# Kernel tuning notes

Hardware: AMD Instinct MI355X
Metric: run time of the kernel (lower is better)

## Reference

```python
import jax, jax.numpy as jnp
import numpy as np

EMBED = 1024
HEAD = 128

def setup_inputs() -> dict:
    key = jax.random.key(0)
    k1, k2, k3, k4 = jax.random.split(key, 4)
    x = jax.random.normal(k1, (8, 2048, EMBED), dtype=jnp.float32)
    s = 1.0 / np.sqrt(EMBED)
    Wk = jax.random.normal(k2, (EMBED, HEAD), dtype=jnp.float32) * s
    Wq = jax.random.normal(k3, (EMBED, HEAD), dtype=jnp.float32) * s
    Wv = jax.random.normal(k4, (EMBED, HEAD), dtype=jnp.float32) * s
    return {"x": x, "Wk": Wk, "Wq": Wq, "Wv": Wv}

def reference(x, Wk, Wq, Wv):
    # x: [B,T,E]; projections: [B,T,H]
    k = x @ Wk
    q = x @ Wq
    v = x @ Wv
    T = x.shape[1]
    # NOTE: original scales by 1/sqrt(embedding_size), not head_size
    scale = 1.0 / jnp.sqrt(jnp.asarray(EMBED, dtype=x.dtype))
    scores = jnp.einsum('bth,bsh->bts', q, k) * scale  # [B,T,T]
    causal = jnp.tril(jnp.ones((T, T), dtype=bool))
    scores = jnp.where(causal, scores, -jnp.inf)
    attn = jax.nn.softmax(scores, axis=-1)
    return jnp.einsum('bts,bsh->bth', attn, v)
```

## Files before the change

kernel.cpp:

```cpp
#include <hip/hip_runtime.h>
#include <math.h>

typedef short bf16x2 __attribute__((ext_vector_type(2)));
typedef short bf16x4 __attribute__((ext_vector_type(4)));
typedef short bf16x8 __attribute__((ext_vector_type(8)));
typedef float f32x4 __attribute__((ext_vector_type(4)));

#define EMBED 1024
#define HEAD 128
#define BATCH 8
#define SEQ 2048

__device__ __forceinline__ short f2bf(float f) {
  union { float f; unsigned u; } v;
  v.f = f;
  unsigned r = v.u + 0x7fffu + ((v.u >> 16) & 1u);
  return (short)(r >> 16);
}

__device__ __forceinline__ void async_copy16(const void* g, void* l) {
#if __has_builtin(__builtin_amdgcn_global_load_lds)
  __builtin_amdgcn_global_load_lds(
      (const __attribute__((address_space(1))) unsigned int*)g,
      (__attribute__((address_space(3))) unsigned int*)l, 16, 0, 0);
#else
  *(f32x4*)l = *(const f32x4*)g;
#endif
}

__global__ __launch_bounds__(256) void wtrans_kernel(
    const float* __restrict__ Wq, const float* __restrict__ Wk,
    const float* __restrict__ Wv, short* __restrict__ WT) {
  __shared__ float tile[32][33];
  int kt = blockIdx.x * 32;
  int ht = blockIdx.y * 32;
  int mtx = blockIdx.z;
  const float* W = (mtx == 0) ? Wq : ((mtx == 1) ? Wk : Wv);
  float scale = (mtx == 0) ? (1.4426950408889634f / 32.0f) : 1.0f;
  int tc = threadIdx.x & 31;
  int tr = threadIdx.x >> 5;
#pragma unroll
  for (int i = 0; i < 4; i++) {
    int r = tr + i * 8;
    tile[r][tc] = W[(size_t)(kt + r) * HEAD + ht + tc];
  }
  __syncthreads();
#pragma unroll
  for (int i = 0; i < 4; i++) {
    int r = tr + i * 8;
    WT[(size_t)(mtx * HEAD + ht + r) * EMBED + kt + tc] = f2bf(tile[tc][r] * scale);
  }
}

__global__ __launch_bounds__(256, 3) void proj_kernel(
    const float* __restrict__ x, const short* __restrict__ WT,
    short* __restrict__ q, short* __restrict__ k, short* __restrict__ vT) {
  __shared__ __align__(16) short As[2][64 * 72];
  __shared__ __align__(16) short Bs[2][64 * 128];
  int tid = threadIdx.x;
  int w = tid >> 6, lane = tid & 63, quad = lane >> 4, sub = lane & 15;
  int mw = w & 1, nw = w >> 1;
  int bx = blockIdx.x;
  int nt = bx % 3;
  int mt = bx / 3;
  int m0 = mt * 64;
  int bb = m0 >> 11;
  int t0 = m0 & 2047;

  int arow = tid >> 2;
  int akq = (tid & 3) * 16;
  const float* xbase = x + (size_t)(m0 + arow) * EMBED + akq;
  int aoff = arow * 72 + akq;

  const short* wsrc[4];
#pragma unroll
  for (int j = 0; j < 4; j++) {
    int cc = j * 256 + tid;
    wsrc[j] = WT + (size_t)(nt * 128 + (cc & 127)) * EMBED + (cc >> 7) * 8;
  }

  f32x4 acc[2][4];
#pragma unroll
  for (int am = 0; am < 2; am++)
#pragma unroll
    for (int an = 0; an < 4; an++) acc[am][an] = (f32x4)(0.0f);

  {
    f32x4 x0 = *(const f32x4*)(xbase + 0);
    f32x4 x1 = *(const f32x4*)(xbase + 4);
    f32x4 x2 = *(const f32x4*)(xbase + 8);
    f32x4 x3 = *(const f32x4*)(xbase + 12);
    bf16x8 w0, w1;
    w0[0]=f2bf(x0[0]); w0[1]=f2bf(x0[1]); w0[2]=f2bf(x0[2]); w0[3]=f2bf(x0[3]);
    w0[4]=f2bf(x1[0]); w0[5]=f2bf(x1[1]); w0[6]=f2bf(x1[2]); w0[7]=f2bf(x1[3]);
    w1[0]=f2bf(x2[0]); w1[1]=f2bf(x2[1]); w1[2]=f2bf(x2[2]); w1[3]=f2bf(x2[3]);
    w1[4]=f2bf(x3[0]); w1[5]=f2bf(x3[1]); w1[6]=f2bf(x3[2]); w1[7]=f2bf(x3[3]);
    *(bf16x8*)&As[0][aoff] = w0;
    *(bf16x8*)&As[0][aoff + 8] = w1;
#pragma unroll
    for (int j = 0; j < 4; j++) async_copy16(wsrc[j], &Bs[0][(j * 256 + tid) * 8]);
  }
  f32x4 xr0 = *(const f32x4*)(xbase + 64);
  f32x4 xr1 = *(const f32x4*)(xbase + 68);
  f32x4 xr2 = *(const f32x4*)(xbase + 72);
  f32x4 xr3 = *(const f32x4*)(xbase + 76);

  for (int it = 0; it < 16; it++) {
    int cur = it & 1;
    __syncthreads();
    if (it < 15) {
      int nxt = cur ^ 1;
      bf16x8 w0, w1;
      w0[0]=f2bf(xr0[0]); w0[1]=f2bf(xr0[1]); w0[2]=f2bf(xr0[2]); w0[3]=f2bf(xr0[3]);
      w0[4]=f2bf(xr1[0]); w0[5]=f2bf(xr1[1]); w0[6]=f2bf(xr1[2]); w0[7]=f2bf(xr1[3]);
      w1[0]=f2bf(xr2[0]); w1[1]=f2bf(xr2[1]); w1[2]=f2bf(xr2[2]); w1[3]=f2bf(xr2[3]);
      w1[4]=f2bf(xr3[0]); w1[5]=f2bf(xr3[1]); w1[6]=f2bf(xr3[2]); w1[7]=f2bf(xr3[3]);
      *(bf16x8*)&As[nxt][aoff] = w0;
      *(bf16x8*)&As[nxt][aoff + 8] = w1;
      int kb1 = (it + 1) * 64;
#pragma unroll
      for (int j = 0; j < 4; j++)
        async_copy16(wsrc[j] + kb1, &Bs[nxt][(j * 256 + tid) * 8]);
      if (it < 14) {
        int kb2 = (it + 2) * 64;
        xr0 = *(const f32x4*)(xbase + kb2);
        xr1 = *(const f32x4*)(xbase + kb2 + 4);
        xr2 = *(const f32x4*)(xbase + kb2 + 8);
        xr3 = *(const f32x4*)(xbase + kb2 + 12);
      }
    }
#pragma unroll
    for (int ks = 0; ks < 2; ks++) {
      bf16x8 a0 = *(const bf16x8*)&As[cur][(mw * 32 + sub) * 72 + ks * 32 + quad * 8];
      bf16x8 a1 = *(const bf16x8*)&As[cur][(mw * 32 + 16 + sub) * 72 + ks * 32 + quad * 8];
#pragma unroll
      for (int an = 0; an < 4; an++) {
        bf16x8 bb = *(const bf16x8*)&Bs[cur][((ks * 4 + quad) * 128 + nw * 64 + an * 16 + sub) * 8];
        acc[0][an] = __builtin_amdgcn_mfma_f32_16x16x32_bf16(a0, bb, acc[0][an], 0, 0, 0);
        acc[1][an] = __builtin_amdgcn_mfma_f32_16x16x32_bf16(a1, bb, acc[1][an], 0, 0, 0);
      }
    }
  }

  if (nt < 2) {
    short* dst = (nt == 0) ? q : k;
#pragma unroll
    for (int am = 0; am < 2; am++)
#pragma unroll
      for (int an = 0; an < 4; an++) {
        int col = nw * 64 + an * 16 + sub;
#pragma unroll
        for (int r = 0; r < 4; r++) {
          int m = m0 + mw * 32 + am * 16 + quad * 4 + r;
          dst[(size_t)m * HEAD + col] = f2bf(acc[am][an][r]);
        }
      }
  } else {
    short* vls = &As[0][0];
    __syncthreads();
#pragma unroll
    for (int am = 0; am < 2; am++)
#pragma unroll
      for (int an = 0; an < 4; an++) {
        int h = nw * 64 + an * 16 + sub;
        int m = mw * 32 + am * 16 + quad * 4;
        bf16x4 pv;
#pragma unroll
        for (int r = 0; r < 4; r++) pv[r] = f2bf(acc[am][an][r]);
        *(bf16x4*)&vls[h * 72 + m] = pv;
      }
    __syncthreads();
    int h = tid >> 1, seg = tid & 1;
    bf16x8 v0 = *(const bf16x8*)&vls[h * 72 + seg * 32];
    bf16x8 v1 = *(const bf16x8*)&vls[h * 72 + seg * 32 + 8];
    bf16x8 v2 = *(const bf16x8*)&vls[h * 72 + seg * 32 + 16];
    bf16x8 v3 = *(const bf16x8*)&vls[h * 72 + seg * 32 + 24];
    short* dp = vT + (size_t)(bb * HEAD + h) * SEQ + t0 + seg * 32;
    *(bf16x8*)(dp) = v0;
    *(bf16x8*)(dp + 8) = v1;
    *(bf16x8*)(dp + 16) = v2;
    *(bf16x8*)(dp + 24) = v3;
  }
}

__global__ __launch_bounds__(256, 4) void attn_kernel(
    const short* __restrict__ q, const short* __restrict__ k,
    const short* __restrict__ vT, float* __restrict__ o_acc,
    float* __restrict__ l_acc) {
  __shared__ __align__(16) short Kb[2][4096];
  __shared__ __align__(16) short Vb[2][4096];
  __shared__ __align__(16) short Pb[4][2][16 * 40];
  int tid = threadIdx.x;
  int w = tid >> 6, lane = tid & 63, quad = lane >> 4, sub = lane & 15;
  int bx = blockIdx.x;
  int b = bx & 7;
  int v = 79 - (bx >> 3);
  int qt, c;
  if (v < 8)       { qt = v;                               c = 0; }
  else if (v < 24) { int i2 = v - 8;  qt = 8  + (i2 >> 1); c = i2 & 1; }
  else if (v < 48) { int i2 = v - 24; qt = 16 + i2 / 3;    c = i2 % 3; }
  else             { int i2 = v - 48; qt = 24 + (i2 >> 2); c = i2 & 3; }
  int q0 = qt * 64;
  int kb0 = c * 512;
  int len = min(512, q0 + 64 - kb0);
  int ntiles = len >> 5;

  const short* kp = k + (size_t)b * SEQ * HEAD;
  const short* vp = vT + (size_t)b * HEAD * SEQ;
  int cc0 = tid, cc1 = tid + 256;

  bf16x8 qf[4];
  const short* qrow = q + (size_t)(b * SEQ + q0 + w * 16 + sub) * HEAD + quad * 8;
#pragma unroll
  for (int kc = 0; kc < 4; kc++) qf[kc] = *(const bf16x8*)(qrow + kc * 32);

  f32x4 o[8];
#pragma unroll
  for (int h = 0; h < 8; h++) o[h] = (f32x4)(0.0f);
  float l[4] = {0.0f, 0.0f, 0.0f, 0.0f};
  int wrow = q0 + w * 16;
  int qrq = wrow + quad * 4;

  async_copy16(kp + (size_t)(kb0 + (cc0 & 31)) * HEAD + (cc0 >> 5) * 8, &Kb[0][cc0 * 8]);
  async_copy16(kp + (size_t)(kb0 + (cc1 & 31)) * HEAD + (cc1 >> 5) * 8, &Kb[0][cc1 * 8]);
  async_copy16(vp + (size_t)(cc0 & 127) * SEQ + kb0 + (cc0 >> 7) * 8, &Vb[0][cc0 * 8]);
  async_copy16(vp + (size_t)(cc1 & 127) * SEQ + kb0 + (cc1 >> 7) * 8, &Vb[0][cc1 * 8]);

  for (int j = 0; j < ntiles; j++) {
    int kb = kb0 + j * 32;
    int cur = j & 1;
    __syncthreads();
    if (j + 1 < ntiles) {
      int nxt = cur ^ 1;
      int kb1 = kb + 32;
      async_copy16(kp + (size_t)(kb1 + (cc0 & 31)) * HEAD + (cc0 >> 5) * 8, &Kb[nxt][cc0 * 8]);
      async_copy16(kp + (size_t)(kb1 + (cc1 & 31)) * HEAD + (cc1 >> 5) * 8, &Kb[nxt][cc1 * 8]);
      async_copy16(vp + (size_t)(cc0 & 127) * SEQ + kb1 + (cc0 >> 7) * 8, &Vb[nxt][cc0 * 8]);
      async_copy16(vp + (size_t)(cc1 & 127) * SEQ + kb1 + (cc1 >> 7) * 8, &Vb[nxt][cc1 * 8]);
    }
    f32x4 s0 = (f32x4)(0.0f), s1 = (f32x4)(0.0f);
#pragma unroll
    for (int kk = 0; kk < 4; kk++) {
      bf16x8 f0 = *(const bf16x8*)&Kb[cur][((kk * 4 + quad) * 32 + sub) * 8];
      bf16x8 f1 = *(const bf16x8*)&Kb[cur][((kk * 4 + quad) * 32 + 16 + sub) * 8];
      s0 = __builtin_amdgcn_mfma_f32_16x16x32_bf16(qf[kk], f0, s0, 0, 0, 0);
      s1 = __builtin_amdgcn_mfma_f32_16x16x32_bf16(qf[kk], f1, s1, 0, 0, 0);
    }
    bool edge = (kb + 31 > wrow);
    float e0[4], e1[4];
#pragma unroll
    for (int r = 0; r < 4; r++) {
      e0[r] = __builtin_amdgcn_exp2f(s0[r]);
      e1[r] = __builtin_amdgcn_exp2f(s1[r]);
    }
    if (edge) {
#pragma unroll
      for (int r = 0; r < 4; r++) {
        if (kb + sub > qrq + r) e0[r] = 0.0f;
        if (kb + 16 + sub > qrq + r) e1[r] = 0.0f;
      }
    }
    short* pw = &Pb[w][cur][0];
#pragma unroll
    for (int r = 0; r < 4; r++) {
      l[r] += e0[r] + e1[r];
      pw[(quad * 4 + r) * 40 + sub] = f2bf(e0[r]);
      pw[(quad * 4 + r) * 40 + sub + 16] = f2bf(e1[r]);
    }
    bf16x8 pa = *(const bf16x8*)&pw[sub * 40 + quad * 8];
#pragma unroll
    for (int h8 = 0; h8 < 8; h8++) {
      bf16x8 vf = *(const bf16x8*)&Vb[cur][(quad * 128 + h8 * 16 + sub) * 8];
      o[h8] = __builtin_amdgcn_mfma_f32_16x16x32_bf16(pa, vf, o[h8], 0, 0, 0);
    }
  }

  float* ob = o_acc + (size_t)(b * SEQ + qrq) * HEAD + sub;
#pragma unroll
  for (int r = 0; r < 4; r++)
#pragma unroll
    for (int h8 = 0; h8 < 8; h8++)
      unsafeAtomicAdd(ob + (size_t)r * HEAD + h8 * 16, o[h8][r]);
#pragma unroll
  for (int r = 0; r < 4; r++) {
#pragma unroll
    for (int off = 1; off < 16; off <<= 1) l[r] += __shfl_xor(l[r], off);
  }
  if (sub == 0) {
#pragma unroll
    for (int r = 0; r < 4; r++)
      unsafeAtomicAdd(&l_acc[b * SEQ + qrq + r], l[r]);
  }
}

__global__ __launch_bounds__(256) void norm_kernel(
    float* __restrict__ o, const float* __restrict__ l_acc) {
  int idx = blockIdx.x * 256 + threadIdx.x;
  f32x4 v = ((const f32x4*)o)[idx];
  float inv = 1.0f / l_acc[idx >> 5];
  v[0] *= inv; v[1] *= inv; v[2] *= inv; v[3] *= inv;
  ((f32x4*)o)[idx] = v;
}

extern "C" void kernel_launch(void* const* d_in, const int* in_sizes, int n_in,
                              void* d_out, int out_size, void* d_ws, size_t ws_size,
                              hipStream_t stream) {
  const float* x  = (const float*)d_in[0];
  const float* Wk = (const float*)d_in[1];
  const float* Wq = (const float*)d_in[2];
  const float* Wv = (const float*)d_in[3];
  char* ws = (char*)d_ws;
  short* WT    = (short*)(ws);
  short* vT    = (short*)(ws + (size_t)1  * (1 << 20));
  short* q     = (short*)(ws + (size_t)5  * (1 << 20));
  short* k     = (short*)(ws + (size_t)9  * (1 << 20));
  float* l_acc = (float*)(ws + (size_t)13 * (1 << 20));
  float* out   = (float*)d_out;

  hipMemsetAsync(out, 0, (size_t)BATCH * SEQ * HEAD * sizeof(float), stream);
  hipMemsetAsync(l_acc, 0, (size_t)BATCH * SEQ * sizeof(float), stream);
  wtrans_kernel<<<dim3(32, 4, 3), 256, 0, stream>>>(Wq, Wk, Wv, WT);
  proj_kernel<<<dim3(768), 256, 0, stream>>>(x, WT, q, k, vT);
  attn_kernel<<<dim3(640), 256, 0, stream>>>(q, k, vT, out, l_acc);
  norm_kernel<<<dim3(2048), 256, 0, stream>>>(out, l_acc);
}
```

Measured before the change: 177.0 us.

## Fuse QKV projection into one wide tile and load V directly from global

The projection kernel now computes all three Q/K/V outputs per 64-row tile, using 512-thread blocks over 384 columns. Each x tile is read and converted to bf16 once instead of three times, at the cost of only 256 blocks at one block per CU and a larger LDS footprint. Separately, the attention kernel drops the LDS staging buffer for V and loads V fragments straight from global memory into registers each iteration. This removes LDS traffic and space but exposes global load latency inside the loop without async prefetch.

```diff
diff --git a/kernel.cpp b/kernel.cpp
--- a/kernel.cpp
+++ b/kernel.cpp
@@ -52,134 +52,111 @@
   }
 }
 
-__global__ __launch_bounds__(256, 3) void proj_kernel(
+__global__ __launch_bounds__(512, 1) void proj_kernel(
     const float* __restrict__ x, const short* __restrict__ WT,
     short* __restrict__ q, short* __restrict__ k, short* __restrict__ vT) {
-  __shared__ __align__(16) short As[2][64 * 72];
-  __shared__ __align__(16) short Bs[2][64 * 128];
+  __shared__ __align__(16) short As[2][512 * 8];
+  __shared__ __align__(16) short Bs[2][3072 * 8];
   int tid = threadIdx.x;
   int w = tid >> 6, lane = tid & 63, quad = lane >> 4, sub = lane & 15;
-  int mw = w & 1, nw = w >> 1;
-  int bx = blockIdx.x;
-  int nt = bx % 3;
-  int mt = bx / 3;
-  int m0 = mt * 64;
-  int bb = m0 >> 11;
-  int t0 = m0 & 2047;
-
-  int arow = tid >> 2;
-  int akq = (tid & 3) * 16;
-  const float* xbase = x + (size_t)(m0 + arow) * EMBED + akq;
-  int aoff = arow * 72 + akq;
-
-  const short* wsrc[4];
-#pragma unroll
-  for (int j = 0; j < 4; j++) {
-    int cc = j * 256 + tid;
-    wsrc[j] = WT + (size_t)(nt * 128 + (cc & 127)) * EMBED + (cc >> 7) * 8;
-  }
-
-  f32x4 acc[2][4];
+  int mw = w >> 2, nw = w & 3;
+  int m0 = blockIdx.x * 64;
+  int bb = m0 >> 11, t0 = m0 & 2047;
+
+  int arow = tid & 63, akq = tid >> 6;
+  const float* xbase = x + (size_t)(m0 + arow) * EMBED + akq * 8;
+
+  const short* wsrc[6];
+  int bdst[6];
+#pragma unroll
+  for (int j = 0; j < 6; j++) {
+    int c = j * 512 + tid;
+    int kq = c / 384, n = c - kq * 384;
+    wsrc[j] = WT + (size_t)n * EMBED + kq * 8;
+    bdst[j] = c * 8;
+  }
+
+  f32x4 acc[2][6];
 #pragma unroll
   for (int am = 0; am < 2; am++)
 #pragma unroll
-    for (int an = 0; an < 4; an++) acc[am][an] = (f32x4)(0.0f);
+    for (int an = 0; an < 6; an++) acc[am][an] = (f32x4)(0.0f);
 
   {
-    f32x4 x0 = *(const f32x4*)(xbase + 0);
+    f32x4 x0 = *(const f32x4*)(xbase);
     f32x4 x1 = *(const f32x4*)(xbase + 4);
-    f32x4 x2 = *(const f32x4*)(xbase + 8);
-    f32x4 x3 = *(const f32x4*)(xbase + 12);
-    bf16x8 w0, w1;
-    w0[0]=f2bf(x0[0]); w0[1]=f2bf(x0[1]); w0[2]=f2bf(x0[2]); w0[3]=f2bf(x0[3]);
-    w0[4]=f2bf(x1[0]); w0[5]=f2bf(x1[1]); w0[6]=f2bf(x1[2]); w0[7]=f2bf(x1[3]);
-    w1[0]=f2bf(x2[0]); w1[1]=f2bf(x2[1]); w1[2]=f2bf(x2[2]); w1[3]=f2bf(x2[3]);
-    w1[4]=f2bf(x3[0]); w1[5]=f2bf(x3[1]); w1[6]=f2bf(x3[2]); w1[7]=f2bf(x3[3]);
-    *(bf16x8*)&As[0][aoff] = w0;
-    *(bf16x8*)&As[0][aoff + 8] = w1;
-#pragma unroll
-    for (int j = 0; j < 4; j++) async_copy16(wsrc[j], &Bs[0][(j * 256 + tid) * 8]);
+    bf16x8 a8;
+    a8[0]=f2bf(x0[0]); a8[1]=f2bf(x0[1]); a8[2]=f2bf(x0[2]); a8[3]=f2bf(x0[3]);
+    a8[4]=f2bf(x1[0]); a8[5]=f2bf(x1[1]); a8[6]=f2bf(x1[2]); a8[7]=f2bf(x1[3]);
+    *(bf16x8*)&As[0][tid * 8] = a8;
+#pragma unroll
+    for (int j = 0; j < 6; j++) async_copy16(wsrc[j], &Bs[0][bdst[j]]);
   }
   f32x4 xr0 = *(const f32x4*)(xbase + 64);
   f32x4 xr1 = *(const f32x4*)(xbase + 68);
-  f32x4 xr2 = *(const f32x4*)(xbase + 72);
-  f32x4 xr3 = *(const f32x4*)(xbase + 76);
 
   for (int it = 0; it < 16; it++) {
     int cur = it & 1;
     __syncthreads();
     if (it < 15) {
       int nxt = cur ^ 1;
-      bf16x8 w0, w1;
-      w0[0]=f2bf(xr0[0]); w0[1]=f2bf(xr0[1]); w0[2]=f2bf(xr0[2]); w0[3]=f2bf(xr0[3]);
-      w0[4]=f2bf(xr1[0]); w0[5]=f2bf(xr1[1]); w0[6]=f2bf(xr1[2]); w0[7]=f2bf(xr1[3]);
-      w1[0]=f2bf(xr2[0]); w1[1]=f2bf(xr2[1]); w1[2]=f2bf(xr2[2]); w1[3]=f2bf(xr2[3]);
-      w1[4]=f2bf(xr3[0]); w1[5]=f2bf(xr3[1]); w1[6]=f2bf(xr3[2]); w1[7]=f2bf(xr3[3]);
-      *(bf16x8*)&As[nxt][aoff] = w0;
-      *(bf16x8*)&As[nxt][aoff + 8] = w1;
+      bf16x8 a8;
+      a8[0]=f2bf(xr0[0]); a8[1]=f2bf(xr0[1]); a8[2]=f2bf(xr0[2]); a8[3]=f2bf(xr0[3]);
+      a8[4]=f2bf(xr1[0]); a8[5]=f2bf(xr1[1]); a8[6]=f2bf(xr1[2]); a8[7]=f2bf(xr1[3]);
+      *(bf16x8*)&As[nxt][tid * 8] = a8;
       int kb1 = (it + 1) * 64;
 #pragma unroll
-      for (int j = 0; j < 4; j++)
-        async_copy16(wsrc[j] + kb1, &Bs[nxt][(j * 256 + tid) * 8]);
+      for (int j = 0; j < 6; j++) async_copy16(wsrc[j] + kb1, &Bs[nxt][bdst[j]]);
       if (it < 14) {
-        int kb2 = (it + 2) * 64;
-        xr0 = *(const f32x4*)(xbase + kb2);
-        xr1 = *(const f32x4*)(xbase + kb2 + 4);
-        xr2 = *(const f32x4*)(xbase + kb2 + 8);
-        xr3 = *(const f32x4*)(xbase + kb2 + 12);
+        xr0 = *(const f32x4*)(xbase + (it + 2) * 64);
+        xr1 = *(const f32x4*)(xbase + (it + 2) * 64 + 4);
       }
     }
 #pragma unroll
     for (int ks = 0; ks < 2; ks++) {
-      bf16x8 a0 = *(const bf16x8*)&As[cur][(mw * 32 + sub) * 72 + ks * 32 + quad * 8];
-      bf16x8 a1 = *(const bf16x8*)&As[cur][(mw * 32 + 16 + sub) * 72 + ks * 32 + quad * 8];
-#pragma unroll
-      for (int an = 0; an < 4; an++) {
-        bf16x8 bb = *(const bf16x8*)&Bs[cur][((ks * 4 + quad) * 128 + nw * 64 + an * 16 + sub) * 8];
-        acc[0][an] = __builtin_amdgcn_mfma_f32_16x16x32_bf16(a0, bb, acc[0][an], 0, 0, 0);
-        acc[1][an] = __builtin_amdgcn_mfma_f32_16x16x32_bf16(a1, bb, acc[1][an], 0, 0, 0);
+      int kq = ks * 4 + quad;
+      bf16x8 a0 = *(const bf16x8*)&As[cur][(kq * 64 + mw * 32 + sub) * 8];
+      bf16x8 a1 = *(const bf16x8*)&As[cur][(kq * 64 + mw * 32 + 16 + sub) * 8];
+#pragma unroll
+      for (int an = 0; an < 6; an++) {
+        bf16x8 b8 = *(const bf16x8*)&Bs[cur][(kq * 384 + nw * 96 + an * 16 + sub) * 8];
+        acc[0][an] = __builtin_amdgcn_mfma_f32_16x16x32_bf16(a0, b8, acc[0][an], 0, 0, 0);
+        acc[1][an] = __builtin_amdgcn_mfma_f32_16x16x32_bf16(a1, b8, acc[1][an], 0, 0, 0);
       }
     }
   }
 
-  if (nt < 2) {
-    short* dst = (nt == 0) ? q : k;
-#pragma unroll
-    for (int am = 0; am < 2; am++)
-#pragma unroll
-      for (int an = 0; an < 4; an++) {
-        int col = nw * 64 + an * 16 + sub;
+  short* vls = &Bs[0][0];
+#pragma unroll
+  for (int am = 0; am < 2; am++)
+#pragma unroll
+    for (int an = 0; an < 6; an++) {
+      int nbt = nw * 6 + an;
+      if (nbt < 16) {
+        short* dst = (nbt < 8) ? q : k;
+        int col = (nbt & 7) * 16 + sub;
 #pragma unroll
         for (int r = 0; r < 4; r++) {
           int m = m0 + mw * 32 + am * 16 + quad * 4 + r;
           dst[(size_t)m * HEAD + col] = f2bf(acc[am][an][r]);
         }
-      }
-  } else {
-    short* vls = &As[0][0];
-    __syncthreads();
-#pragma unroll
-    for (int am = 0; am < 2; am++)
-#pragma unroll
-      for (int an = 0; an < 4; an++) {
-        int h = nw * 64 + an * 16 + sub;
+      } else {
+        int h = (nbt - 16) * 16 + sub;
         int m = mw * 32 + am * 16 + quad * 4;
         bf16x4 pv;
 #pragma unroll
         for (int r = 0; r < 4; r++) pv[r] = f2bf(acc[am][an][r]);
         *(bf16x4*)&vls[h * 72 + m] = pv;
       }
-    __syncthreads();
-    int h = tid >> 1, seg = tid & 1;
-    bf16x8 v0 = *(const bf16x8*)&vls[h * 72 + seg * 32];
-    bf16x8 v1 = *(const bf16x8*)&vls[h * 72 + seg * 32 + 8];
-    bf16x8 v2 = *(const bf16x8*)&vls[h * 72 + seg * 32 + 16];
-    bf16x8 v3 = *(const bf16x8*)&vls[h * 72 + seg * 32 + 24];
-    short* dp = vT + (size_t)(bb * HEAD + h) * SEQ + t0 + seg * 32;
-    *(bf16x8*)(dp) = v0;
+    }
+  __syncthreads();
+  {
+    int h = tid >> 2, seg = tid & 3;
+    bf16x8 v0 = *(const bf16x8*)&vls[h * 72 + seg * 16];
+    bf16x8 v1 = *(const bf16x8*)&vls[h * 72 + seg * 16 + 8];
+    short* dp = vT + (size_t)(bb * HEAD + h) * SEQ + t0 + seg * 16;
+    *(bf16x8*)dp = v0;
     *(bf16x8*)(dp + 8) = v1;
-    *(bf16x8*)(dp + 16) = v2;
-    *(bf16x8*)(dp + 24) = v3;
   }
 }
 
@@ -188,7 +165,6 @@
     const short* __restrict__ vT, float* __restrict__ o_acc,
     float* __restrict__ l_acc) {
   __shared__ __align__(16) short Kb[2][4096];
-  __shared__ __align__(16) short Vb[2][4096];
   __shared__ __align__(16) short Pb[4][2][16 * 40];
   int tid = threadIdx.x;
   int w = tid >> 6, lane = tid & 63, quad = lane >> 4, sub = lane & 15;
@@ -206,7 +182,7 @@
   int ntiles = len >> 5;
 
   const short* kp = k + (size_t)b * SEQ * HEAD;
-  const short* vp = vT + (size_t)b * HEAD * SEQ;
+  const short* vbase = vT + (size_t)(b * HEAD + sub) * SEQ + quad * 8;
   int cc0 = tid, cc1 = tid + 256;
 
   bf16x8 qf[4];
@@ -223,8 +199,6 @@
 
   async_copy16(kp + (size_t)(kb0 + (cc0 & 31)) * HEAD + (cc0 >> 5) * 8, &Kb[0][cc0 * 8]);
   async_copy16(kp + (size_t)(kb0 + (cc1 & 31)) * HEAD + (cc1 >> 5) * 8, &Kb[0][cc1 * 8]);
-  async_copy16(vp + (size_t)(cc0 & 127) * SEQ + kb0 + (cc0 >> 7) * 8, &Vb[0][cc0 * 8]);
-  async_copy16(vp + (size_t)(cc1 & 127) * SEQ + kb0 + (cc1 >> 7) * 8, &Vb[0][cc1 * 8]);
 
   for (int j = 0; j < ntiles; j++) {
     int kb = kb0 + j * 32;
@@ -235,9 +209,11 @@
       int kb1 = kb + 32;
       async_copy16(kp + (size_t)(kb1 + (cc0 & 31)) * HEAD + (cc0 >> 5) * 8, &Kb[nxt][cc0 * 8]);
       async_copy16(kp + (size_t)(kb1 + (cc1 & 31)) * HEAD + (cc1 >> 5) * 8, &Kb[nxt][cc1 * 8]);
-      async_copy16(vp + (size_t)(cc0 & 127) * SEQ + kb1 + (cc0 >> 7) * 8, &Vb[nxt][cc0 * 8]);
-      async_copy16(vp + (size_t)(cc1 & 127) * SEQ + kb1 + (cc1 >> 7) * 8, &Vb[nxt][cc1 * 8]);
-    }
+    }
+    bf16x8 vf[8];
+#pragma unroll
+    for (int h8 = 0; h8 < 8; h8++)
+      vf[h8] = *(const bf16x8*)(vbase + (size_t)(h8 * 16) * SEQ + kb);
     f32x4 s0 = (f32x4)(0.0f), s1 = (f32x4)(0.0f);
 #pragma unroll
     for (int kk = 0; kk < 4; kk++) {
@@ -269,10 +245,8 @@
     }
     bf16x8 pa = *(const bf16x8*)&pw[sub * 40 + quad * 8];
 #pragma unroll
-    for (int h8 = 0; h8 < 8; h8++) {
-      bf16x8 vf = *(const bf16x8*)&Vb[cur][(quad * 128 + h8 * 16 + sub) * 8];
-      o[h8] = __builtin_amdgcn_mfma_f32_16x16x32_bf16(pa, vf, o[h8], 0, 0, 0);
-    }
+    for (int h8 = 0; h8 < 8; h8++)
+      o[h8] = __builtin_amdgcn_mfma_f32_16x16x32_bf16(pa, vf[h8], o[h8], 0, 0, 0);
   }
 
   float* ob = o_acc + (size_t)(b * SEQ + qrq) * HEAD + sub;
@@ -320,7 +294,7 @@
   hipMemsetAsync(out, 0, (size_t)BATCH * SEQ * HEAD * sizeof(float), stream);
   hipMemsetAsync(l_acc, 0, (size_t)BATCH * SEQ * sizeof(float), stream);
   wtrans_kernel<<<dim3(32, 4, 3), 256, 0, stream>>>(Wq, Wk, Wv, WT);
-  proj_kernel<<<dim3(768), 256, 0, stream>>>(x, WT, q, k, vT);
+  proj_kernel<<<dim3(256), 512, 0, stream>>>(x, WT, q, k, vT);
   attn_kernel<<<dim3(640), 256, 0, stream>>>(q, k, vT, out, l_acc);
   norm_kernel<<<dim3(2048), 256, 0, stream>>>(out, l_acc);
 }
```

After: 203.9 us. 15.2% more time.

## Split attention KV range into 256-key chunks and regroup projection blocks

Applied to the files above, without the earlier changes.

The attention kernel now splits each query tile's causal key range into 256-key chunks instead of 512, which raises the grid from 640 to 1152 blocks. A closed-form group decode with up to 8 chunks per group replaces the old piecewise mapping, aiming at better load balance and fuller CU occupancy on the causal triangle. The P staging buffer loses its double-buffer dimension, cutting shared memory per block. The projection kernel reorders blocks so that 8 consecutive row tiles share each weight column tile, to improve L2 reuse of the weights. The trade-off is more partial-output atomic traffic into o_acc/l_acc and reuse of a single P buffer per wave across iterations.

```diff
diff --git a/kernel.cpp b/kernel.cpp
--- a/kernel.cpp
+++ b/kernel.cpp
@@ -61,9 +61,11 @@
   int w = tid >> 6, lane = tid & 63, quad = lane >> 4, sub = lane & 15;
   int mw = w & 1, nw = w >> 1;
   int bx = blockIdx.x;
-  int nt = bx % 3;
-  int mt = bx / 3;
-  int m0 = mt * 64;
+  int sup = bx / 24;
+  int rem = bx - sup * 24;
+  int nt = rem >> 3;
+  int s = sup * 8 + (rem & 7);
+  int m0 = s * 64;
   int bb = m0 >> 11;
   int t0 = m0 & 2047;
 
@@ -135,9 +137,9 @@
       bf16x8 a1 = *(const bf16x8*)&As[cur][(mw * 32 + 16 + sub) * 72 + ks * 32 + quad * 8];
 #pragma unroll
       for (int an = 0; an < 4; an++) {
-        bf16x8 bb = *(const bf16x8*)&Bs[cur][((ks * 4 + quad) * 128 + nw * 64 + an * 16 + sub) * 8];
-        acc[0][an] = __builtin_amdgcn_mfma_f32_16x16x32_bf16(a0, bb, acc[0][an], 0, 0, 0);
-        acc[1][an] = __builtin_amdgcn_mfma_f32_16x16x32_bf16(a1, bb, acc[1][an], 0, 0, 0);
+        bf16x8 bb8 = *(const bf16x8*)&Bs[cur][((ks * 4 + quad) * 128 + nw * 64 + an * 16 + sub) * 8];
+        acc[0][an] = __builtin_amdgcn_mfma_f32_16x16x32_bf16(a0, bb8, acc[0][an], 0, 0, 0);
+        acc[1][an] = __builtin_amdgcn_mfma_f32_16x16x32_bf16(a1, bb8, acc[1][an], 0, 0, 0);
       }
     }
   }
@@ -189,20 +191,24 @@
     float* __restrict__ l_acc) {
   __shared__ __align__(16) short Kb[2][4096];
   __shared__ __align__(16) short Vb[2][4096];
-  __shared__ __align__(16) short Pb[4][2][16 * 40];
+  __shared__ __align__(16) short Pb[4][16 * 40];
   int tid = threadIdx.x;
   int w = tid >> 6, lane = tid & 63, quad = lane >> 4, sub = lane & 15;
   int bx = blockIdx.x;
   int b = bx & 7;
-  int v = 79 - (bx >> 3);
-  int qt, c;
-  if (v < 8)       { qt = v;                               c = 0; }
-  else if (v < 24) { int i2 = v - 8;  qt = 8  + (i2 >> 1); c = i2 & 1; }
-  else if (v < 48) { int i2 = v - 24; qt = 16 + i2 / 3;    c = i2 % 3; }
-  else             { int i2 = v - 48; qt = 24 + (i2 >> 2); c = i2 & 3; }
+  int v = 143 - (bx >> 3);
+  int g = 0;
+#pragma unroll
+  for (int gg = 1; gg < 8; gg++)
+    if (v >= 2 * gg * (gg + 1)) g = gg;
+  int r0 = v - 2 * g * (g + 1);
+  int den = g + 1;
+  int qi = r0 / den;
+  int c = r0 - qi * den;
+  int qt = 4 * g + qi;
   int q0 = qt * 64;
-  int kb0 = c * 512;
-  int len = min(512, q0 + 64 - kb0);
+  int kb0 = c * 256;
+  int len = min(256, q0 + 64 - kb0);
   int ntiles = len >> 5;
 
   const short* kp = k + (size_t)b * SEQ * HEAD;
@@ -260,7 +266,7 @@
         if (kb + 16 + sub > qrq + r) e1[r] = 0.0f;
       }
     }
-    short* pw = &Pb[w][cur][0];
+    short* pw = &Pb[w][0];
 #pragma unroll
     for (int r = 0; r < 4; r++) {
       l[r] += e0[r] + e1[r];
@@ -321,6 +327,6 @@
   hipMemsetAsync(l_acc, 0, (size_t)BATCH * SEQ * sizeof(float), stream);
   wtrans_kernel<<<dim3(32, 4, 3), 256, 0, stream>>>(Wq, Wk, Wv, WT);
   proj_kernel<<<dim3(768), 256, 0, stream>>>(x, WT, q, k, vT);
-  attn_kernel<<<dim3(640), 256, 0, stream>>>(q, k, vT, out, l_acc);
+  attn_kernel<<<dim3(1152), 256, 0, stream>>>(q, k, vT, out, l_acc);
   norm_kernel<<<dim3(2048), 256, 0, stream>>>(out, l_acc);
 }
```

New measurement: 187.0 us. +5.6%, slower.
